# Performance work log

Hardware: AMD Instinct MI355X
Metric: run time of the kernel (lower is better)

The kernel has to match this reference:

```python
import jax, jax.numpy as jnp
import numpy as np

N, F_IN, HID, E, B, C = 50000, 128, 256, 1600000, 64, 10

def setup_inputs() -> dict:
    key = jax.random.key(0)
    ks = jax.random.split(key, 20)
    def lin(k, out_d, in_d):
        s = 1.0 / np.sqrt(in_d)
        return jax.random.uniform(k, (out_d, in_d), jnp.float32, -s, s)
    inp = {
        'x': jax.random.normal(ks[0], (N, F_IN), jnp.float32),
        'edge_index': jax.random.randint(ks[1], (2, E), 0, N, jnp.int64),
        'batch': jnp.sort(jax.random.randint(ks[2], (N,), 0, B, jnp.int64)),
        # SAGEConv layer 1: lin_l (neighbors, with bias) + lin_r (root)
        'W1l': lin(ks[3], HID, F_IN), 'b1l': jnp.zeros((HID,), jnp.float32), 'W1r': lin(ks[4], HID, F_IN),
        # SAGEConv layers 2,3
        'W2l': lin(ks[5], HID, HID), 'b2l': jnp.zeros((HID,), jnp.float32), 'W2r': lin(ks[6], HID, HID),
        'W3l': lin(ks[7], HID, HID), 'b3l': jnp.zeros((HID,), jnp.float32), 'W3r': lin(ks[8], HID, HID),
        # GlobalAttention gate: Linear(hidden, 1)
        'Wg': lin(ks[9], 1, HID), 'bg': jnp.zeros((1,), jnp.float32),
        # MLP head
        'Wl1': lin(ks[10], HID, HID), 'bl1': jnp.zeros((HID,), jnp.float32),
        'Wl2': lin(ks[11], C, HID), 'bl2': jnp.zeros((C,), jnp.float32),
    }
    return inp

def _sage(x, Wl, bl, Wr, src, dst):
    # mean aggregation of source-node features at destination nodes
    deg = jax.ops.segment_sum(jnp.ones((src.shape[0],), x.dtype), dst, N)
    agg = jax.ops.segment_sum(x[src], dst, N) / jnp.clip(deg, 1.0)[:, None]
    return agg @ Wl.T + bl + x @ Wr.T

def reference(x, edge_index, batch, W1l, b1l, W1r, W2l, b2l, W2r, W3l, b3l, W3r, Wg, bg, Wl1, bl1, Wl2, bl2):
    src, dst = edge_index[0], edge_index[1]
    h = jax.nn.relu(_sage(x, W1l, b1l, W1r, src, dst))
    h = jax.nn.relu(_sage(h, W2l, b2l, W2r, src, dst))
    h = jax.nn.relu(_sage(h, W3l, b3l, W3r, src, dst))
    # GlobalAttention pooling: segment softmax over gate scores, weighted sum
    gate = (h @ Wg.T + bg)[:, 0]                                  # [N]
    m = jax.ops.segment_max(gate, batch, B)                       # [B]
    e = jnp.exp(gate - m[batch])
    s = jax.ops.segment_sum(e, batch, B)                          # [B]
    a = e / s[batch]
    pooled = jax.ops.segment_sum(a[:, None] * h, batch, B)        # [B, HID]
    out = jax.nn.relu(pooled @ Wl1.T + bl1)
    # dropout p=0.5 is identity in eval mode
    out = out @ Wl2.T + bl2
    return jax.nn.log_softmax(out, axis=-1)
```

## Files before the change

### kernel.cpp

```cpp
#include <hip/hip_runtime.h>

#define NN 50000
#define FIN 128
#define HID 256
#define NE 1600000
#define NBG 64
#define NC 10
#define NBINS ((NN + 255) >> 8)

typedef short bf16x8 __attribute__((ext_vector_type(8)));
typedef float f32x4 __attribute__((ext_vector_type(4)));
typedef float floatx2 __attribute__((ext_vector_type(2)));

static __device__ __forceinline__ ushort f2b(float f){
  unsigned u = __float_as_uint(f);
  unsigned r = (u + 0x7FFFu + ((u >> 16) & 1u)) >> 16;
  return (ushort)r;
}
static __device__ __forceinline__ float b2f(ushort u){
  return __uint_as_float(((unsigned)u) << 16);
}

__global__ void k_init(int* __restrict__ bincnt, float* __restrict__ pooled){
  int i = blockIdx.x*256 + threadIdx.x;
  if (i < 256) bincnt[i] = 0;
  if (i < NBG*HID) pooled[i] = 0.f;
}

__global__ void k_xb(const float* __restrict__ x, ushort* __restrict__ xb){
  int i = blockIdx.x*256 + threadIdx.x;
  if (i >= NN*FIN/4) return;
  float4 v = *(const float4*)(x + (size_t)i*4);
  ushort4 o; o.x=f2b(v.x); o.y=f2b(v.y); o.z=f2b(v.z); o.w=f2b(v.w);
  *(ushort4*)(xb + (size_t)i*4) = o;
}

__global__ void k_wcat(const float* __restrict__ Wl, const float* __restrict__ Wr,
                       int F, ushort* __restrict__ Wc){
  int F2 = 2*F;
  int i = blockIdx.x*256 + threadIdx.x;
  if (i >= HID*F2) return;
  int n = i / F2, k = i % F2;
  float v = (k < F) ? Wl[(size_t)n*F + k] : Wr[(size_t)n*F + (k-F)];
  Wc[i] = f2b(v);
}

__global__ __launch_bounds__(256) void k_binhist(const int* __restrict__ dst,
                                                 int* __restrict__ bincnt){
  __shared__ int lh[NBINS];
  int t = threadIdx.x;
  for (int i=t; i<NBINS; i+=256) lh[i]=0;
  __syncthreads();
  long e0 = (long)blockIdx.x * 4096;
  #pragma unroll
  for (int k=0;k<16;++k){
    long e = e0 + k*256 + t;
    if (e < NE) atomicAdd(&lh[dst[e] >> 8], 1);
  }
  __syncthreads();
  for (int i=t; i<NBINS; i+=256)
    if (lh[i]) atomicAdd(&bincnt[i], lh[i]);
}

__global__ void k_scanbins(const int* __restrict__ bincnt, int* __restrict__ binoff,
                           int* __restrict__ gcur){
  __shared__ int buf[2][256];
  int t = threadIdx.x;
  int v = (t < NBINS) ? bincnt[t] : 0;
  buf[0][t] = v; __syncthreads();
  int pp = 0;
  for (int off=1; off<256; off<<=1){
    int nv = buf[pp][t];
    if (t >= off) nv += buf[pp][t-off];
    buf[pp^1][t] = nv; __syncthreads(); pp ^= 1;
  }
  int excl = buf[pp][t] - v;
  if (t < NBINS){ binoff[t] = excl; gcur[t] = excl; }
  if (t == 0) binoff[NBINS] = NE;
}

__global__ __launch_bounds__(256) void k_pass1(const int* __restrict__ src,
                                               const int* __restrict__ dst,
                                               int* __restrict__ gcur,
                                               unsigned* __restrict__ ebin){
  __shared__ int lhist[NBINS];
  __shared__ int lbase[NBINS];
  int t = threadIdx.x;
  long e0 = (long)blockIdx.x * 4096;
  for (int i=t; i<NBINS; i+=256) lhist[i]=0;
  __syncthreads();
  unsigned pk[16]; int bn[16]; int rk[16];
  #pragma unroll
  for (int k=0;k<16;++k){
    long e = e0 + k*256 + t;
    bn[k] = -1;
    if (e < NE){
      int d = dst[e];
      int s = src[e];
      bn[k] = d >> 8;
      pk[k] = (unsigned)s | ((unsigned)(d & 255) << 24);
      rk[k] = atomicAdd(&lhist[bn[k]], 1);
    }
  }
  __syncthreads();
  for (int i=t; i<NBINS; i+=256)
    lbase[i] = atomicAdd(&gcur[i], lhist[i]);
  __syncthreads();
  #pragma unroll
  for (int k=0;k<16;++k)
    if (bn[k] >= 0) ebin[lbase[bn[k]] + rk[k]] = pk[k];
}

__global__ __launch_bounds__(256) void k_pass2(const unsigned* __restrict__ ebin,
                                               const int* __restrict__ binoff,
                                               int* __restrict__ rowp,
                                               int* __restrict__ deg,
                                               float* __restrict__ invd,
                                               int* __restrict__ srcs){
  __shared__ int cnt[256];
  __shared__ int buf[2][256];
  __shared__ int cur[256];
  int b = blockIdx.x, t = threadIdx.x;
  int d0 = b << 8;
  int st = binoff[b], en = binoff[b+1];
  cnt[t] = 0;
  __syncthreads();
  for (int i = st + t; i < en; i += 256)
    atomicAdd(&cnt[ebin[i] >> 24], 1);
  __syncthreads();
  int v = cnt[t];
  buf[0][t] = v; __syncthreads();
  int pp = 0;
  for (int off=1; off<256; off<<=1){
    int nv = buf[pp][t];
    if (t >= off) nv += buf[pp][t-off];
    buf[pp^1][t] = nv; __syncthreads(); pp ^= 1;
  }
  int excl = st + buf[pp][t] - v;
  if (d0 + t < NN){
    rowp[d0 + t] = excl;
    deg[d0 + t] = v;
    invd[d0 + t] = 1.0f / (float)max(v, 1);
  }
  cur[t] = excl;
  __syncthreads();
  for (int i = st + t; i < en; i += 256){
    unsigned p = ebin[i];
    int doff = p >> 24;
    int pos = atomicAdd(&cur[doff], 1);
    srcs[pos] = (int)(p & 0xFFFFFFu);
  }
}

template<int F>
__global__ void k_agg(const ushort* __restrict__ x, const int* __restrict__ srcs,
                      const int* __restrict__ rowp, const int* __restrict__ deg,
                      const float* __restrict__ invd, ushort* __restrict__ out){
  constexpr int LPR = F/8;
  constexpr int EPI = 64/LPR;
  int w = blockIdx.x*4 + (threadIdx.x>>6);
  int lane = threadIdx.x & 63;
  if (w >= NN) return;
  int st = rowp[w], d = deg[w];
  int grp = lane / LPR;
  int fo  = (lane % LPR)*8;
  float acc[8];
  #pragma unroll
  for (int v=0;v<8;++v) acc[v]=0.f;

  auto accum = [&](uint4 u){
    acc[0] += __uint_as_float(u.x<<16); acc[1] += __uint_as_float(u.x & 0xFFFF0000u);
    acc[2] += __uint_as_float(u.y<<16); acc[3] += __uint_as_float(u.y & 0xFFFF0000u);
    acc[4] += __uint_as_float(u.z<<16); acc[5] += __uint_as_float(u.z & 0xFFFF0000u);
    acc[6] += __uint_as_float(u.w<<16); acc[7] += __uint_as_float(u.w & 0xFFFF0000u);
  };

  int j = 0;
  for (; j + 4*EPI <= d; j += 4*EPI){
    int i0 = srcs[st + j + grp];
    int i1 = srcs[st + j + EPI + grp];
    int i2 = srcs[st + j + 2*EPI + grp];
    int i3 = srcs[st + j + 3*EPI + grp];
    uint4 u0 = *(const uint4*)(x + (size_t)i0*F + fo);
    uint4 u1 = *(const uint4*)(x + (size_t)i1*F + fo);
    uint4 u2 = *(const uint4*)(x + (size_t)i2*F + fo);
    uint4 u3 = *(const uint4*)(x + (size_t)i3*F + fo);
    accum(u0); accum(u1); accum(u2); accum(u3);
  }
  for (; j < d; j += EPI){
    int jj = j + grp;
    if (jj < d){
      int i0 = srcs[st + jj];
      uint4 u0 = *(const uint4*)(x + (size_t)i0*F + fo);
      accum(u0);
    }
  }
  #pragma unroll
  for (int off = LPR; off < 64; off <<= 1){
    #pragma unroll
    for (int v=0;v<8;++v) acc[v] += __shfl_xor(acc[v], off);
  }
  if (grp == 0){
    float sc = invd[w];
    uint4 o;
    o.x = (unsigned)f2b(acc[0]*sc) | ((unsigned)f2b(acc[1]*sc)<<16);
    o.y = (unsigned)f2b(acc[2]*sc) | ((unsigned)f2b(acc[3]*sc)<<16);
    o.z = (unsigned)f2b(acc[4]*sc) | ((unsigned)f2b(acc[5]*sc)<<16);
    o.w = (unsigned)f2b(acc[6]*sc) | ((unsigned)f2b(acc[7]*sc)<<16);
    *(uint4*)(out + (size_t)w*F + fo) = o;
  }
}

__global__ void k_agg8(const unsigned* __restrict__ x8, const int* __restrict__ srcs,
                       const int* __restrict__ rowp, const int* __restrict__ deg,
                       const float* __restrict__ invd, ushort* __restrict__ out){
  int w = blockIdx.x*4 + (threadIdx.x>>6);
  int lane = threadIdx.x & 63;
  if (w >= NN) return;
  int st = rowp[w], d = deg[w];
  int grp = lane >> 4;
  int sub = lane & 15;
  const uint4* xr = (const uint4*)x8;
  float acc[16];
  #pragma unroll
  for (int v=0;v<16;++v) acc[v]=0.f;

  auto accum = [&](uint4 u){
    floatx2 p;
    p = __builtin_amdgcn_cvt_pk_f32_fp8(u.x, false); acc[0]+=p.x;  acc[1]+=p.y;
    p = __builtin_amdgcn_cvt_pk_f32_fp8(u.x, true);  acc[2]+=p.x;  acc[3]+=p.y;
    p = __builtin_amdgcn_cvt_pk_f32_fp8(u.y, false); acc[4]+=p.x;  acc[5]+=p.y;
    p = __builtin_amdgcn_cvt_pk_f32_fp8(u.y, true);  acc[6]+=p.x;  acc[7]+=p.y;
    p = __builtin_amdgcn_cvt_pk_f32_fp8(u.z, false); acc[8]+=p.x;  acc[9]+=p.y;
    p = __builtin_amdgcn_cvt_pk_f32_fp8(u.z, true);  acc[10]+=p.x; acc[11]+=p.y;
    p = __builtin_amdgcn_cvt_pk_f32_fp8(u.w, false); acc[12]+=p.x; acc[13]+=p.y;
    p = __builtin_amdgcn_cvt_pk_f32_fp8(u.w, true);  acc[14]+=p.x; acc[15]+=p.y;
  };

  int j = 0;
  for (; j + 16 <= d; j += 16){
    int i0 = srcs[st + j + grp];
    int i1 = srcs[st + j + 4 + grp];
    int i2 = srcs[st + j + 8 + grp];
    int i3 = srcs[st + j + 12 + grp];
    uint4 u0 = xr[(size_t)i0*16 + sub];
    uint4 u1 = xr[(size_t)i1*16 + sub];
    uint4 u2 = xr[(size_t)i2*16 + sub];
    uint4 u3 = xr[(size_t)i3*16 + sub];
    accum(u0); accum(u1); accum(u2); accum(u3);
  }
  for (; j < d; j += 4){
    int jj = j + grp;
    if (jj < d){
      int i0 = srcs[st + jj];
      uint4 u0 = xr[(size_t)i0*16 + sub];
      accum(u0);
    }
  }
  #pragma unroll
  for (int off = 16; off < 64; off <<= 1){
    #pragma unroll
    for (int v=0;v<16;++v) acc[v] += __shfl_xor(acc[v], off);
  }
  if (grp == 0){
    float sc = invd[w];
    uint4 o1, o2;
    o1.x = (unsigned)f2b(acc[0]*sc)  | ((unsigned)f2b(acc[1]*sc)<<16);
    o1.y = (unsigned)f2b(acc[2]*sc)  | ((unsigned)f2b(acc[3]*sc)<<16);
    o1.z = (unsigned)f2b(acc[4]*sc)  | ((unsigned)f2b(acc[5]*sc)<<16);
    o1.w = (unsigned)f2b(acc[6]*sc)  | ((unsigned)f2b(acc[7]*sc)<<16);
    o2.x = (unsigned)f2b(acc[8]*sc)  | ((unsigned)f2b(acc[9]*sc)<<16);
    o2.y = (unsigned)f2b(acc[10]*sc) | ((unsigned)f2b(acc[11]*sc)<<16);
    o2.z = (unsigned)f2b(acc[12]*sc) | ((unsigned)f2b(acc[13]*sc)<<16);
    o2.w = (unsigned)f2b(acc[14]*sc) | ((unsigned)f2b(acc[15]*sc)<<16);
    ushort* op = out + (size_t)w*HID + sub*16;
    *(uint4*)op = o1;
    *(uint4*)(op + 8) = o2;
  }
}

#define LDT 72
__global__ __launch_bounds__(512) void k_gemm(
    const ushort* __restrict__ A1, int ldA1,
    const ushort* __restrict__ A2, int ldA2,
    const ushort* __restrict__ Wc, int F2,
    const float* __restrict__ bias, ushort* __restrict__ out,
    unsigned* __restrict__ out8, int M)
{
  __shared__ ushort As[128*LDT];
  __shared__ ushort Bs[256*LDT];
  int t = threadIdx.x;
  int l = t & 63;
  int wv = t >> 6;
  int wr = wv >> 2, wc = wv & 3;
  int m0 = blockIdx.x * 128;
  int F = F2 >> 1;
  f32x4 acc[4][4];
  #pragma unroll
  for (int a=0;a<4;++a)
  #pragma unroll
  for (int b=0;b<4;++b) acc[a][b] = (f32x4){0.f,0.f,0.f,0.f};

  int nsteps = F2/64;
  for (int s=0; s<nsteps; ++s){
    int kk = s*64;
    const ushort* src; int ld, kkl;
    if (kk < F){ src = A1; ld = ldA1; kkl = kk; }
    else       { src = A2; ld = ldA2; kkl = kk - F; }
    uint4 av[2];
    int arow[2], ack[2];
    #pragma unroll
    for (int i=0;i<2;++i){
      int c = t*2 + i;
      arow[i] = c >> 3; ack[i] = c & 7;
      int m = m0 + arow[i];
      av[i] = make_uint4(0u,0u,0u,0u);
      if (m < M) av[i] = *(const uint4*)(src + (size_t)m*ld + kkl + ack[i]*8);
    }
    uint4 bv[4];
    int brow[4], bck[4];
    #pragma unroll
    for (int i=0;i<4;++i){
      int c = t*4 + i;
      brow[i] = c >> 3; bck[i] = c & 7;
      bv[i] = *(const uint4*)(Wc + (size_t)brow[i]*F2 + kk + bck[i]*8);
    }
    #pragma unroll
    for (int i=0;i<2;++i)
      *(uint4*)&As[arow[i]*LDT + ack[i]*8] = av[i];
    #pragma unroll
    for (int i=0;i<4;++i)
      *(uint4*)&Bs[brow[i]*LDT + bck[i]*8] = bv[i];
    __syncthreads();

    #pragma unroll
    for (int ks=0; ks<2; ++ks){
      bf16x8 af[4], bf[4];
      int ko = ks*32 + (l>>4)*8;
      #pragma unroll
      for (int mf=0; mf<4; ++mf)
        af[mf] = *(bf16x8*)&As[(wr*64 + mf*16 + (l&15))*LDT + ko];
      #pragma unroll
      for (int nf=0; nf<4; ++nf)
        bf[nf] = *(bf16x8*)&Bs[(wc*64 + nf*16 + (l&15))*LDT + ko];
      #pragma unroll
      for (int mf=0; mf<4; ++mf)
      #pragma unroll
      for (int nf=0; nf<4; ++nf)
        acc[mf][nf] = __builtin_amdgcn_mfma_f32_16x16x32_bf16(bf[nf], af[mf], acc[mf][nf], 0, 0, 0);
    }
    __syncthreads();
  }

  #pragma unroll
  for (int mf=0; mf<4; ++mf){
    int m = m0 + wr*64 + mf*16 + (l&15);
    if (m >= M) continue;
    #pragma unroll
    for (int nf=0; nf<4; ++nf){
      int ncol = wc*64 + nf*16 + (l>>4)*4;
      float4 bb = *(const float4*)&bias[ncol];
      float v0 = fmaxf(acc[mf][nf][0] + bb.x, 0.f);
      float v1 = fmaxf(acc[mf][nf][1] + bb.y, 0.f);
      float v2 = fmaxf(acc[mf][nf][2] + bb.z, 0.f);
      float v3 = fmaxf(acc[mf][nf][3] + bb.w, 0.f);
      ushort4 o;
      o.x = f2b(v0); o.y = f2b(v1); o.z = f2b(v2); o.w = f2b(v3);
      *(ushort4*)(out + (size_t)m*HID + ncol) = o;
      if (out8){
        int r = __builtin_amdgcn_cvt_pk_fp8_f32(v0, v1, 0, false);
        r = __builtin_amdgcn_cvt_pk_fp8_f32(v2, v3, r, true);
        out8[(size_t)m*(HID/4) + (ncol>>2)] = (unsigned)r;
      }
    }
  }
}

__global__ void k_gate(const ushort* __restrict__ h, const float* __restrict__ Wg,
                       const float* __restrict__ bg, float* __restrict__ gate){
  int w = blockIdx.x*4 + (threadIdx.x>>6);
  int lane = threadIdx.x & 63;
  if (w >= NN) return;
  uint2 u = *(const uint2*)(h + (size_t)w*HID + lane*4);
  float4 wg = *(const float4*)(Wg + lane*4);
  float d = __uint_as_float(u.x<<16)*wg.x + __uint_as_float(u.x&0xFFFF0000u)*wg.y
          + __uint_as_float(u.y<<16)*wg.z + __uint_as_float(u.y&0xFFFF0000u)*wg.w;
  #pragma unroll
  for (int o=32;o>0;o>>=1) d += __shfl_down(d, o);
  if (lane==0) gate[w] = d + bg[0];
}

__global__ void k_seg(const int* __restrict__ batch, int* __restrict__ starts){
  int b = threadIdx.x;
  if (b > NBG) return;
  int lo = 0, hi = NN;
  while (lo < hi){ int mid = (lo+hi)>>1; if (batch[mid] < b) lo = mid+1; else hi = mid; }
  starts[b] = lo;
}

__global__ void k_msum(const float* __restrict__ gate, const int* __restrict__ starts,
                       float* __restrict__ m, float* __restrict__ s){
  __shared__ float sm[256];
  int b = blockIdx.x, t = threadIdx.x;
  int st = starts[b], en = starts[b+1];
  float mx = -3.0e38f;
  for (int i = st + t; i < en; i += 256) mx = fmaxf(mx, gate[i]);
  sm[t] = mx; __syncthreads();
  for (int o=128;o>0;o>>=1){ if (t<o) sm[t]=fmaxf(sm[t],sm[t+o]); __syncthreads(); }
  float M = sm[0]; __syncthreads();
  float su = 0.f;
  for (int i = st + t; i < en; i += 256) su += expf(gate[i]-M);
  sm[t] = su; __syncthreads();
  for (int o=128;o>0;o>>=1){ if (t<o) sm[t]+=sm[t+o]; __syncthreads(); }
  if (t==0){ m[b]=M; s[b]=sm[0]; }
}

__global__ __launch_bounds__(256) void k_pool(const ushort* __restrict__ h,
                                              const float* __restrict__ gate,
                                              const int* __restrict__ batch,
                                              const float* __restrict__ m,
                                              const float* __restrict__ s,
                                              float* __restrict__ pooled){
  __shared__ float sa[128];
  __shared__ int sb[128];
  int t = threadIdx.x;
  int i0 = blockIdx.x*128;
  if (t < 128){
    int i = i0 + t;
    if (i < NN){
      int b = batch[i];
      sb[t] = b;
      sa[t] = expf(gate[i] - m[b]) / s[b];
    } else sb[t] = -1;
  }
  __syncthreads();
  int strm = t >> 6;
  int f = (t & 63) * 4;
  int j0 = strm * 32;
  float a0=0.f, a1=0.f, a2=0.f, a3=0.f;
  int bcur = sb[j0];
  for (int j = j0; j < j0 + 32; ++j){
    int i = i0 + j;
    if (i >= NN) break;
    int b = sb[j];
    if (b != bcur){
      if (bcur >= 0){
        atomicAdd(&pooled[bcur*HID + f + 0], a0);
        atomicAdd(&pooled[bcur*HID + f + 1], a1);
        atomicAdd(&pooled[bcur*HID + f + 2], a2);
        atomicAdd(&pooled[bcur*HID + f + 3], a3);
      }
      a0=a1=a2=a3=0.f; bcur = b;
    }
    ushort4 hv = *(const ushort4*)(h + (size_t)i*HID + f);
    float c = sa[j];
    a0 = fmaf(c, b2f(hv.x), a0);
    a1 = fmaf(c, b2f(hv.y), a1);
    a2 = fmaf(c, b2f(hv.z), a2);
    a3 = fmaf(c, b2f(hv.w), a3);
  }
  if (bcur >= 0){
    atomicAdd(&pooled[bcur*HID + f + 0], a0);
    atomicAdd(&pooled[bcur*HID + f + 1], a1);
    atomicAdd(&pooled[bcur*HID + f + 2], a2);
    atomicAdd(&pooled[bcur*HID + f + 3], a3);
  }
}

__global__ void k_head(const float* __restrict__ pooled, const float* __restrict__ Wl1,
                       const float* __restrict__ bl1, const float* __restrict__ Wl2,
                       const float* __restrict__ bl2, float* __restrict__ out){
  __shared__ float pr[256]; __shared__ float o1[256]; __shared__ float lg[16];
  int b = blockIdx.x, t = threadIdx.x;
  pr[t] = pooled[b*HID + t];
  __syncthreads();
  float a = bl1[t];
  const float* wr = Wl1 + (size_t)t*HID;
  #pragma unroll 4
  for (int k=0;k<HID;k+=4){
    float4 w4 = *(const float4*)(wr + k);
    a += pr[k]*w4.x + pr[k+1]*w4.y + pr[k+2]*w4.z + pr[k+3]*w4.w;
  }
  o1[t] = fmaxf(a, 0.f);
  __syncthreads();
  if (t < NC){
    float a2 = bl2[t];
    const float* w2 = Wl2 + (size_t)t*HID;
    for (int k=0;k<HID;++k) a2 += o1[k]*w2[k];
    lg[t] = a2;
  }
  __syncthreads();
  if (t == 0){
    float mx = lg[0];
    for (int c2=1;c2<NC;++c2) mx = fmaxf(mx, lg[c2]);
    float se = 0.f;
    for (int c2=0;c2<NC;++c2) se += expf(lg[c2]-mx);
    float lse = mx + logf(se);
    for (int c2=0;c2<NC;++c2) out[b*NC + c2] = lg[c2] - lse;
  }
}

extern "C" void kernel_launch(void* const* d_in, const int* in_sizes, int n_in,
                              void* d_out, int out_size, void* d_ws, size_t ws_size,
                              hipStream_t stream){
  const float* x   = (const float*)d_in[0];
  const int*   ei  = (const int*)d_in[1];
  const int*   bat = (const int*)d_in[2];
  const float* W1l = (const float*)d_in[3];
  const float* b1l = (const float*)d_in[4];
  const float* W1r = (const float*)d_in[5];
  const float* W2l = (const float*)d_in[6];
  const float* b2l = (const float*)d_in[7];
  const float* W2r = (const float*)d_in[8];
  const float* W3l = (const float*)d_in[9];
  const float* b3l = (const float*)d_in[10];
  const float* W3r = (const float*)d_in[11];
  const float* Wg  = (const float*)d_in[12];
  const float* bg  = (const float*)d_in[13];
  const float* Wl1 = (const float*)d_in[14];
  const float* bl1 = (const float*)d_in[15];
  const float* Wl2 = (const float*)d_in[16];
  const float* bl2 = (const float*)d_in[17];
  const int* srcI = ei;
  const int* dstI = ei + NE;
  float* out = (float*)d_out;

  char* w = (char*)d_ws;
  auto take = [&](size_t bytes)->char*{
    char* p = w; w += (bytes + 255) & ~(size_t)255; return p;
  };
  int*      deg    = (int*)take((size_t)NN*4);
  float*    invd   = (float*)take((size_t)NN*4);
  int*      rowp   = (int*)take((size_t)NN*4);
  int*      gcur   = (int*)take(256*4);
  int*      bincnt = (int*)take(256*4);
  int*      binoff = (int*)take(256*4);
  int*      srcs   = (int*)take((size_t)NE*4);
  unsigned* ebin   = (unsigned*)take((size_t)NE*4);
  float*    gate   = (float*)take((size_t)NN*4);
  int*      starts = (int*)take(128*4);
  float*    m      = (float*)take(64*4);
  float*    s      = (float*)take(64*4);
  float*    pooled = (float*)take(64*256*4);
  ushort*   xb     = (ushort*)take((size_t)NN*FIN*2);
  ushort*   Wc1    = (ushort*)take((size_t)HID*2*FIN*2);
  ushort*   Wc2    = (ushort*)take((size_t)HID*2*HID*2);
  ushort*   Wc3    = (ushort*)take((size_t)HID*2*HID*2);
  ushort*   AG     = (ushort*)take((size_t)NN*HID*2);
  ushort*   HB     = (ushort*)take((size_t)NN*HID*2);
  unsigned* H8     = (unsigned*)take((size_t)NN*HID);

  k_init<<<(NN+255)/256, 256, 0, stream>>>(bincnt, pooled);
  k_xb<<<(NN*FIN/4+255)/256, 256, 0, stream>>>(x, xb);
  k_wcat<<<(HID*2*FIN+255)/256, 256, 0, stream>>>(W1l, W1r, FIN, Wc1);
  k_wcat<<<(HID*2*HID+255)/256, 256, 0, stream>>>(W2l, W2r, HID, Wc2);
  k_wcat<<<(HID*2*HID+255)/256, 256, 0, stream>>>(W3l, W3r, HID, Wc3);
  k_binhist<<<(NE + 4095)/4096, 256, 0, stream>>>(dstI, bincnt);
  k_scanbins<<<1, 256, 0, stream>>>(bincnt, binoff, gcur);
  k_pass1<<<(NE + 4095)/4096, 256, 0, stream>>>(srcI, dstI, gcur, ebin);
  k_pass2<<<NBINS, 256, 0, stream>>>(ebin, binoff, rowp, deg, invd, srcs);

  int gblocks = (NN + 127)/128;
  k_agg<128><<<(NN+3)/4, 256, 0, stream>>>(xb, srcs, rowp, deg, invd, AG);
  k_gemm<<<gblocks, 512, 0, stream>>>(AG, FIN, xb, FIN, Wc1, 2*FIN, b1l, HB, H8, NN);
  k_agg8<<<(NN+3)/4, 256, 0, stream>>>(H8, srcs, rowp, deg, invd, AG);
  k_gemm<<<gblocks, 512, 0, stream>>>(AG, HID, HB, HID, Wc2, 2*HID, b2l, AG, H8, NN);
  k_agg8<<<(NN+3)/4, 256, 0, stream>>>(H8, srcs, rowp, deg, invd, HB);
  k_gemm<<<gblocks, 512, 0, stream>>>(HB, HID, AG, HID, Wc3, 2*HID, b3l, HB, (unsigned*)nullptr, NN);

  k_gate<<<(NN+3)/4, 256, 0, stream>>>(HB, Wg, bg, gate);
  k_seg<<<1, 128, 0, stream>>>(bat, starts);
  k_msum<<<NBG, 256, 0, stream>>>(gate, starts, m, s);
  k_pool<<<(NN+127)/128, 256, 0, stream>>>(HB, gate, bat, m, s, pooled);
  k_head<<<NBG, 256, 0, stream>>>(pooled, Wl1, bl1, Wl2, bl2, out);
}
```

Before: 487.1 us.

## Use FP8 gather for layer-1 aggregation, fuse gate into last GEMM, drop seg kernel

The input conversion kernel now also writes an FP8 copy of x, so layer-1 neighbor aggregation gathers FP8 rows through a templated k_agg8 instead of BF16 rows. This halves the gather bytes for that layer, at the cost of lower precision in the layer-1 aggregate. The gate dot product moves into the epilogue of the third GEMM through a shared-memory cross-wave reduction, which removes the separate gate kernel and a re-read of H. The segment-start kernel is dropped, and each k_msum block now binary-searches its own graph bounds in the batch array.

```diff
diff --git a/kernel.cpp b/kernel.cpp
--- a/kernel.cpp
+++ b/kernel.cpp
@@ -27,12 +27,23 @@
   if (i < NBG*HID) pooled[i] = 0.f;
 }
 
-__global__ void k_xb(const float* __restrict__ x, ushort* __restrict__ xb){
+__global__ void k_xb(const float* __restrict__ x, ushort* __restrict__ xb,
+                     unsigned* __restrict__ x8){
   int i = blockIdx.x*256 + threadIdx.x;
-  if (i >= NN*FIN/4) return;
-  float4 v = *(const float4*)(x + (size_t)i*4);
-  ushort4 o; o.x=f2b(v.x); o.y=f2b(v.y); o.z=f2b(v.z); o.w=f2b(v.w);
-  *(ushort4*)(xb + (size_t)i*4) = o;
+  if (i >= NN*FIN/8) return;
+  float4 a = *(const float4*)(x + (size_t)i*8);
+  float4 b = *(const float4*)(x + (size_t)i*8 + 4);
+  ushort4 o1, o2;
+  o1.x=f2b(a.x); o1.y=f2b(a.y); o1.z=f2b(a.z); o1.w=f2b(a.w);
+  o2.x=f2b(b.x); o2.y=f2b(b.y); o2.z=f2b(b.z); o2.w=f2b(b.w);
+  *(ushort4*)(xb + (size_t)i*8) = o1;
+  *(ushort4*)(xb + (size_t)i*8 + 4) = o2;
+  int r0 = __builtin_amdgcn_cvt_pk_fp8_f32(a.x, a.y, 0, false);
+  r0 = __builtin_amdgcn_cvt_pk_fp8_f32(a.z, a.w, r0, true);
+  int r1 = __builtin_amdgcn_cvt_pk_fp8_f32(b.x, b.y, 0, false);
+  r1 = __builtin_amdgcn_cvt_pk_fp8_f32(b.z, b.w, r1, true);
+  uint2 o; o.x = (unsigned)r0; o.y = (unsigned)r1;
+  *(uint2*)(x8 + (size_t)i*2) = o;
 }
 
 __global__ void k_wcat(const float* __restrict__ Wl, const float* __restrict__ Wr,
@@ -153,127 +164,73 @@
 }
 
 template<int F>
-__global__ void k_agg(const ushort* __restrict__ x, const int* __restrict__ srcs,
-                      const int* __restrict__ rowp, const int* __restrict__ deg,
-                      const float* __restrict__ invd, ushort* __restrict__ out){
-  constexpr int LPR = F/8;
-  constexpr int EPI = 64/LPR;
+__global__ void k_agg8(const unsigned* __restrict__ x8, const int* __restrict__ srcs,
+                       const int* __restrict__ rowp, const int* __restrict__ deg,
+                       const float* __restrict__ invd, ushort* __restrict__ out){
+  constexpr int LPR = F/16;
+  constexpr int EPG = 64/LPR;
   int w = blockIdx.x*4 + (threadIdx.x>>6);
   int lane = threadIdx.x & 63;
   if (w >= NN) return;
   int st = rowp[w], d = deg[w];
   int grp = lane / LPR;
-  int fo  = (lane % LPR)*8;
-  float acc[8];
-  #pragma unroll
-  for (int v=0;v<8;++v) acc[v]=0.f;
+  int sub = lane % LPR;
+  const uint4* xr = (const uint4*)x8;
+  floatx2 acc[8];
+  #pragma unroll
+  for (int v=0;v<8;++v) acc[v] = (floatx2){0.f,0.f};
 
   auto accum = [&](uint4 u){
-    acc[0] += __uint_as_float(u.x<<16); acc[1] += __uint_as_float(u.x & 0xFFFF0000u);
-    acc[2] += __uint_as_float(u.y<<16); acc[3] += __uint_as_float(u.y & 0xFFFF0000u);
-    acc[4] += __uint_as_float(u.z<<16); acc[5] += __uint_as_float(u.z & 0xFFFF0000u);
-    acc[6] += __uint_as_float(u.w<<16); acc[7] += __uint_as_float(u.w & 0xFFFF0000u);
+    acc[0] += __builtin_amdgcn_cvt_pk_f32_fp8(u.x, false);
+    acc[1] += __builtin_amdgcn_cvt_pk_f32_fp8(u.x, true);
+    acc[2] += __builtin_amdgcn_cvt_pk_f32_fp8(u.y, false);
+    acc[3] += __builtin_amdgcn_cvt_pk_f32_fp8(u.y, true);
+    acc[4] += __builtin_amdgcn_cvt_pk_f32_fp8(u.z, false);
+    acc[5] += __builtin_amdgcn_cvt_pk_f32_fp8(u.z, true);
+    acc[6] += __builtin_amdgcn_cvt_pk_f32_fp8(u.w, false);
+    acc[7] += __builtin_amdgcn_cvt_pk_f32_fp8(u.w, true);
   };
 
   int j = 0;
-  for (; j + 4*EPI <= d; j += 4*EPI){
+  for (; j + 4*EPG <= d; j += 4*EPG){
     int i0 = srcs[st + j + grp];
-    int i1 = srcs[st + j + EPI + grp];
-    int i2 = srcs[st + j + 2*EPI + grp];
-    int i3 = srcs[st + j + 3*EPI + grp];
-    uint4 u0 = *(const uint4*)(x + (size_t)i0*F + fo);
-    uint4 u1 = *(const uint4*)(x + (size_t)i1*F + fo);
-    uint4 u2 = *(const uint4*)(x + (size_t)i2*F + fo);
-    uint4 u3 = *(const uint4*)(x + (size_t)i3*F + fo);
+    int i1 = srcs[st + j + EPG + grp];
+    int i2 = srcs[st + j + 2*EPG + grp];
+    int i3 = srcs[st + j + 3*EPG + grp];
+    uint4 u0 = xr[(size_t)i0*LPR + sub];
+    uint4 u1 = xr[(size_t)i1*LPR + sub];
+    uint4 u2 = xr[(size_t)i2*LPR + sub];
+    uint4 u3 = xr[(size_t)i3*LPR + sub];
     accum(u0); accum(u1); accum(u2); accum(u3);
   }
-  for (; j < d; j += EPI){
+  for (; j < d; j += EPG){
     int jj = j + grp;
     if (jj < d){
       int i0 = srcs[st + jj];
-      uint4 u0 = *(const uint4*)(x + (size_t)i0*F + fo);
+      uint4 u0 = xr[(size_t)i0*LPR + sub];
       accum(u0);
     }
   }
   #pragma unroll
   for (int off = LPR; off < 64; off <<= 1){
     #pragma unroll
-    for (int v=0;v<8;++v) acc[v] += __shfl_xor(acc[v], off);
-  }
-  if (grp == 0){
-    float sc = invd[w];
-    uint4 o;
-    o.x = (unsigned)f2b(acc[0]*sc) | ((unsigned)f2b(acc[1]*sc)<<16);
-    o.y = (unsigned)f2b(acc[2]*sc) | ((unsigned)f2b(acc[3]*sc)<<16);
-    o.z = (unsigned)f2b(acc[4]*sc) | ((unsigned)f2b(acc[5]*sc)<<16);
-    o.w = (unsigned)f2b(acc[6]*sc) | ((unsigned)f2b(acc[7]*sc)<<16);
-    *(uint4*)(out + (size_t)w*F + fo) = o;
-  }
-}
-
-__global__ void k_agg8(const unsigned* __restrict__ x8, const int* __restrict__ srcs,
-                       const int* __restrict__ rowp, const int* __restrict__ deg,
-                       const float* __restrict__ invd, ushort* __restrict__ out){
-  int w = blockIdx.x*4 + (threadIdx.x>>6);
-  int lane = threadIdx.x & 63;
-  if (w >= NN) return;
-  int st = rowp[w], d = deg[w];
-  int grp = lane >> 4;
-  int sub = lane & 15;
-  const uint4* xr = (const uint4*)x8;
-  float acc[16];
-  #pragma unroll
-  for (int v=0;v<16;++v) acc[v]=0.f;
-
-  auto accum = [&](uint4 u){
-    floatx2 p;
-    p = __builtin_amdgcn_cvt_pk_f32_fp8(u.x, false); acc[0]+=p.x;  acc[1]+=p.y;
-    p = __builtin_amdgcn_cvt_pk_f32_fp8(u.x, true);  acc[2]+=p.x;  acc[3]+=p.y;
-    p = __builtin_amdgcn_cvt_pk_f32_fp8(u.y, false); acc[4]+=p.x;  acc[5]+=p.y;
-    p = __builtin_amdgcn_cvt_pk_f32_fp8(u.y, true);  acc[6]+=p.x;  acc[7]+=p.y;
-    p = __builtin_amdgcn_cvt_pk_f32_fp8(u.z, false); acc[8]+=p.x;  acc[9]+=p.y;
-    p = __builtin_amdgcn_cvt_pk_f32_fp8(u.z, true);  acc[10]+=p.x; acc[11]+=p.y;
-    p = __builtin_amdgcn_cvt_pk_f32_fp8(u.w, false); acc[12]+=p.x; acc[13]+=p.y;
-    p = __builtin_amdgcn_cvt_pk_f32_fp8(u.w, true);  acc[14]+=p.x; acc[15]+=p.y;
-  };
-
-  int j = 0;
-  for (; j + 16 <= d; j += 16){
-    int i0 = srcs[st + j + grp];
-    int i1 = srcs[st + j + 4 + grp];
-    int i2 = srcs[st + j + 8 + grp];
-    int i3 = srcs[st + j + 12 + grp];
-    uint4 u0 = xr[(size_t)i0*16 + sub];
-    uint4 u1 = xr[(size_t)i1*16 + sub];
-    uint4 u2 = xr[(size_t)i2*16 + sub];
-    uint4 u3 = xr[(size_t)i3*16 + sub];
-    accum(u0); accum(u1); accum(u2); accum(u3);
-  }
-  for (; j < d; j += 4){
-    int jj = j + grp;
-    if (jj < d){
-      int i0 = srcs[st + jj];
-      uint4 u0 = xr[(size_t)i0*16 + sub];
-      accum(u0);
-    }
-  }
-  #pragma unroll
-  for (int off = 16; off < 64; off <<= 1){
-    #pragma unroll
-    for (int v=0;v<16;++v) acc[v] += __shfl_xor(acc[v], off);
+    for (int v=0;v<8;++v){
+      acc[v].x += __shfl_xor(acc[v].x, off);
+      acc[v].y += __shfl_xor(acc[v].y, off);
+    }
   }
   if (grp == 0){
     float sc = invd[w];
     uint4 o1, o2;
-    o1.x = (unsigned)f2b(acc[0]*sc)  | ((unsigned)f2b(acc[1]*sc)<<16);
-    o1.y = (unsigned)f2b(acc[2]*sc)  | ((unsigned)f2b(acc[3]*sc)<<16);
-    o1.z = (unsigned)f2b(acc[4]*sc)  | ((unsigned)f2b(acc[5]*sc)<<16);
-    o1.w = (unsigned)f2b(acc[6]*sc)  | ((unsigned)f2b(acc[7]*sc)<<16);
-    o2.x = (unsigned)f2b(acc[8]*sc)  | ((unsigned)f2b(acc[9]*sc)<<16);
-    o2.y = (unsigned)f2b(acc[10]*sc) | ((unsigned)f2b(acc[11]*sc)<<16);
-    o2.z = (unsigned)f2b(acc[12]*sc) | ((unsigned)f2b(acc[13]*sc)<<16);
-    o2.w = (unsigned)f2b(acc[14]*sc) | ((unsigned)f2b(acc[15]*sc)<<16);
-    ushort* op = out + (size_t)w*HID + sub*16;
+    o1.x = (unsigned)f2b(acc[0].x*sc) | ((unsigned)f2b(acc[0].y*sc)<<16);
+    o1.y = (unsigned)f2b(acc[1].x*sc) | ((unsigned)f2b(acc[1].y*sc)<<16);
+    o1.z = (unsigned)f2b(acc[2].x*sc) | ((unsigned)f2b(acc[2].y*sc)<<16);
+    o1.w = (unsigned)f2b(acc[3].x*sc) | ((unsigned)f2b(acc[3].y*sc)<<16);
+    o2.x = (unsigned)f2b(acc[4].x*sc) | ((unsigned)f2b(acc[4].y*sc)<<16);
+    o2.y = (unsigned)f2b(acc[5].x*sc) | ((unsigned)f2b(acc[5].y*sc)<<16);
+    o2.z = (unsigned)f2b(acc[6].x*sc) | ((unsigned)f2b(acc[6].y*sc)<<16);
+    o2.w = (unsigned)f2b(acc[7].x*sc) | ((unsigned)f2b(acc[7].y*sc)<<16);
+    ushort* op = out + (size_t)w*F + sub*16;
     *(uint4*)op = o1;
     *(uint4*)(op + 8) = o2;
   }
@@ -285,10 +242,13 @@
     const ushort* __restrict__ A2, int ldA2,
     const ushort* __restrict__ Wc, int F2,
     const float* __restrict__ bias, ushort* __restrict__ out,
-    unsigned* __restrict__ out8, int M)
+    unsigned* __restrict__ out8,
+    const float* __restrict__ Wg, const float* __restrict__ bg,
+    float* __restrict__ gateOut, int M)
 {
   __shared__ ushort As[128*LDT];
   __shared__ ushort Bs[256*LDT];
+  __shared__ float gl[128][4];
   int t = threadIdx.x;
   int l = t & 63;
   int wv = t >> 6;
@@ -352,6 +312,7 @@
     __syncthreads();
   }
 
+  float gp[4] = {0.f, 0.f, 0.f, 0.f};
   #pragma unroll
   for (int mf=0; mf<4; ++mf){
     int m = m0 + wr*64 + mf*16 + (l&15);
@@ -372,37 +333,39 @@
         r = __builtin_amdgcn_cvt_pk_fp8_f32(v2, v3, r, true);
         out8[(size_t)m*(HID/4) + (ncol>>2)] = (unsigned)r;
       }
-    }
-  }
-}
-
-__global__ void k_gate(const ushort* __restrict__ h, const float* __restrict__ Wg,
-                       const float* __restrict__ bg, float* __restrict__ gate){
-  int w = blockIdx.x*4 + (threadIdx.x>>6);
-  int lane = threadIdx.x & 63;
-  if (w >= NN) return;
-  uint2 u = *(const uint2*)(h + (size_t)w*HID + lane*4);
-  float4 wg = *(const float4*)(Wg + lane*4);
-  float d = __uint_as_float(u.x<<16)*wg.x + __uint_as_float(u.x&0xFFFF0000u)*wg.y
-          + __uint_as_float(u.y<<16)*wg.z + __uint_as_float(u.y&0xFFFF0000u)*wg.w;
-  #pragma unroll
-  for (int o=32;o>0;o>>=1) d += __shfl_down(d, o);
-  if (lane==0) gate[w] = d + bg[0];
-}
-
-__global__ void k_seg(const int* __restrict__ batch, int* __restrict__ starts){
-  int b = threadIdx.x;
-  if (b > NBG) return;
-  int lo = 0, hi = NN;
-  while (lo < hi){ int mid = (lo+hi)>>1; if (batch[mid] < b) lo = mid+1; else hi = mid; }
-  starts[b] = lo;
-}
-
-__global__ void k_msum(const float* __restrict__ gate, const int* __restrict__ starts,
+      if (gateOut){
+        float4 wgv = *(const float4*)&Wg[ncol];
+        gp[mf] += v0*wgv.x + v1*wgv.y + v2*wgv.z + v3*wgv.w;
+      }
+    }
+  }
+  if (gateOut){
+    #pragma unroll
+    for (int mf=0; mf<4; ++mf){
+      float g = gp[mf];
+      g += __shfl_xor(g, 16);
+      g += __shfl_xor(g, 32);
+      if ((l >> 4) == 0) gl[wr*64 + mf*16 + (l&15)][wc] = g;
+    }
+    __syncthreads();
+    if (t < 128){
+      int m = m0 + t;
+      if (m < M)
+        gateOut[m] = gl[t][0] + gl[t][1] + gl[t][2] + gl[t][3] + bg[0];
+    }
+  }
+}
+
+__global__ void k_msum(const float* __restrict__ gate, const int* __restrict__ batch,
                        float* __restrict__ m, float* __restrict__ s){
   __shared__ float sm[256];
   int b = blockIdx.x, t = threadIdx.x;
-  int st = starts[b], en = starts[b+1];
+  int lo = 0, hi = NN;
+  while (lo < hi){ int mid = (lo+hi)>>1; if (batch[mid] < b) lo = mid+1; else hi = mid; }
+  int st = lo;
+  hi = NN;
+  while (lo < hi){ int mid = (lo+hi)>>1; if (batch[mid] < b+1) lo = mid+1; else hi = mid; }
+  int en = lo;
   float mx = -3.0e38f;
   for (int i = st + t; i < en; i += 256) mx = fmaxf(mx, gate[i]);
   sm[t] = mx; __syncthreads();
@@ -538,11 +501,11 @@
   int*      srcs   = (int*)take((size_t)NE*4);
   unsigned* ebin   = (unsigned*)take((size_t)NE*4);
   float*    gate   = (float*)take((size_t)NN*4);
-  int*      starts = (int*)take(128*4);
   float*    m      = (float*)take(64*4);
   float*    s      = (float*)take(64*4);
   float*    pooled = (float*)take(64*256*4);
   ushort*   xb     = (ushort*)take((size_t)NN*FIN*2);
+  unsigned* X8     = (unsigned*)take((size_t)NN*FIN);
   ushort*   Wc1    = (ushort*)take((size_t)HID*2*FIN*2);
   ushort*   Wc2    = (ushort*)take((size_t)HID*2*HID*2);
   ushort*   Wc3    = (ushort*)take((size_t)HID*2*HID*2);
@@ -551,7 +514,7 @@
   unsigned* H8     = (unsigned*)take((size_t)NN*HID);
 
   k_init<<<(NN+255)/256, 256, 0, stream>>>(bincnt, pooled);
-  k_xb<<<(NN*FIN/4+255)/256, 256, 0, stream>>>(x, xb);
+  k_xb<<<(NN*FIN/8+255)/256, 256, 0, stream>>>(x, xb, X8);
   k_wcat<<<(HID*2*FIN+255)/256, 256, 0, stream>>>(W1l, W1r, FIN, Wc1);
   k_wcat<<<(HID*2*HID+255)/256, 256, 0, stream>>>(W2l, W2r, HID, Wc2);
   k_wcat<<<(HID*2*HID+255)/256, 256, 0, stream>>>(W3l, W3r, HID, Wc3);
@@ -561,16 +524,17 @@
   k_pass2<<<NBINS, 256, 0, stream>>>(ebin, binoff, rowp, deg, invd, srcs);
 
   int gblocks = (NN + 127)/128;
-  k_agg<128><<<(NN+3)/4, 256, 0, stream>>>(xb, srcs, rowp, deg, invd, AG);
-  k_gemm<<<gblocks, 512, 0, stream>>>(AG, FIN, xb, FIN, Wc1, 2*FIN, b1l, HB, H8, NN);
-  k_agg8<<<(NN+3)/4, 256, 0, stream>>>(H8, srcs, rowp, deg, invd, AG);
-  k_gemm<<<gblocks, 512, 0, stream>>>(AG, HID, HB, HID, Wc2, 2*HID, b2l, AG, H8, NN);
-  k_agg8<<<(NN+3)/4, 256, 0, stream>>>(H8, srcs, rowp, deg, invd, HB);
-  k_gemm<<<gblocks, 512, 0, stream>>>(HB, HID, AG, HID, Wc3, 2*HID, b3l, HB, (unsigned*)nullptr, NN);
-
-  k_gate<<<(NN+3)/4, 256, 0, stream>>>(HB, Wg, bg, gate);
-  k_seg<<<1, 128, 0, stream>>>(bat, starts);
-  k_msum<<<NBG, 256, 0, stream>>>(gate, starts, m, s);
+  k_agg8<FIN><<<(NN+3)/4, 256, 0, stream>>>(X8, srcs, rowp, deg, invd, AG);
+  k_gemm<<<gblocks, 512, 0, stream>>>(AG, FIN, xb, FIN, Wc1, 2*FIN, b1l, HB, H8,
+                                      nullptr, nullptr, nullptr, NN);
+  k_agg8<HID><<<(NN+3)/4, 256, 0, stream>>>(H8, srcs, rowp, deg, invd, AG);
+  k_gemm<<<gblocks, 512, 0, stream>>>(AG, HID, HB, HID, Wc2, 2*HID, b2l, AG, H8,
+                                      nullptr, nullptr, nullptr, NN);
+  k_agg8<HID><<<(NN+3)/4, 256, 0, stream>>>(H8, srcs, rowp, deg, invd, HB);
+  k_gemm<<<gblocks, 512, 0, stream>>>(HB, HID, AG, HID, Wc3, 2*HID, b3l, HB,
+                                      (unsigned*)nullptr, Wg, bg, gate, NN);
+
+  k_msum<<<NBG, 256, 0, stream>>>(gate, bat, m, s);
   k_pool<<<(NN+127)/128, 256, 0, stream>>>(HB, gate, bat, m, s, pooled);
   k_head<<<NBG, 256, 0, stream>>>(pooled, Wl1, bl1, Wl2, bl2, out);
 }
```

Measured after the change: 473.5 us. -2.8%, faster.
